# Kernel tuning notes

Measured on AMD Instinct MI355X. Metric: run time of the kernel, lower is better.

## Reference

```python
import jax, jax.numpy as jnp
import numpy as np

VOCAB = 10000
HID = 256

def setup_inputs() -> dict:
    key = jax.random.key(0)
    ks = jax.random.split(key, 7)
    B, T = 64, 64
    input_data = jax.random.randint(ks[0], (B, T), 0, VOCAB, dtype=jnp.int32)
    targets = jax.random.randint(ks[1], (B, T), 0, VOCAB, dtype=jnp.int32)
    # Xavier-ish scaled params
    E = jax.random.normal(ks[2], (VOCAB, HID), dtype=jnp.float32) * (1.0 / np.sqrt(HID))
    W_lstm = jax.random.normal(ks[3], (2 * HID, 4 * HID), dtype=jnp.float32) * (1.0 / np.sqrt(2 * HID))
    b_lstm = jnp.zeros((4 * HID,), dtype=jnp.float32)
    W_dense = jax.random.normal(ks[4], (HID, VOCAB), dtype=jnp.float32) * (1.0 / np.sqrt(HID))
    b_dense = jnp.zeros((VOCAB,), dtype=jnp.float32)
    return {"input_data": input_data, "targets": targets, "E": E,
            "W_lstm": W_lstm, "b_lstm": b_lstm, "W_dense": W_dense, "b_dense": b_dense}

def lstm_scan(xs, W, b, h0, c0):
    # xs: [T, B, H] time-major. TF LSTMCell: gates = [x,h]@W + b, order i,j,f,o, forget_bias=1.0
    def step(carry, x):
        h, c = carry
        gates = jnp.concatenate([x, h], axis=-1) @ W + b  # [B, 4H]
        i, j, f, o = jnp.split(gates, 4, axis=-1)
        c_new = jax.nn.sigmoid(f + 1.0) * c + jax.nn.sigmoid(i) * jnp.tanh(j)
        h_new = jax.nn.sigmoid(o) * jnp.tanh(c_new)
        return (h_new, c_new), h_new
    (hT, cT), hs = jax.lax.scan(step, (h0, c0), xs)
    return hs, (hT, cT)

def reference(input_data, targets, E, W_lstm, b_lstm, W_dense, b_dense):
    B, T = input_data.shape
    inputs = E[input_data]                       # [B, T, H] embedding lookup (no dropout: eval)
    xs = jnp.transpose(inputs, (1, 0, 2))        # [T, B, H]
    h0 = jnp.zeros((B, HID), dtype=E.dtype)
    c0 = jnp.zeros((B, HID), dtype=E.dtype)
    hs, _ = lstm_scan(xs, W_lstm, b_lstm, h0, c0)  # [T, B, H]
    outputs = jnp.transpose(hs, (1, 0, 2))       # [B, T, H]
    logits = outputs @ W_dense + b_dense         # [B, T, V]
    logp = jax.nn.log_softmax(logits, axis=-1)
    ce = -jnp.take_along_axis(logp, targets[..., None].astype(jnp.int32), axis=-1)[..., 0]  # [B, T]
    perplexity = jnp.exp(ce)                     # elementwise, as in add_loss_op
    return perplexity
```

## Files before the change

### kernel.cpp

```cpp
#include <hip/hip_runtime.h>
#include <math.h>

#define VOCABN 10000
#define HIDN   256
#define GATES  1024
#define BN     64
#define TN     64
#define BT     4096
#define NCT    625

typedef unsigned int       u32;
typedef unsigned short     u16;
typedef unsigned long long u64;
typedef float v4f __attribute__((ext_vector_type(4)));
typedef short v8s __attribute__((ext_vector_type(8)));

__device__ __forceinline__ float bf2f(u16 u) {
    return __uint_as_float(((u32)u) << 16);
}
__device__ __forceinline__ u16 f2bf(float f) {
    u32 u = __float_as_uint(f);
    u += 0x7FFFu + ((u >> 16) & 1u);
    return (u16)(u >> 16);
}
__device__ __forceinline__ float fast_sigmoid(float x) {
    return 1.0f / (1.0f + __expf(-x));
}
__device__ __forceinline__ float fast_tanh(float x) {
    float e = __expf(-2.0f * fabsf(x));
    float t = (1.0f - e) / (1.0f + e);
    return copysignf(t, x);
}
__device__ __forceinline__ u64 llc_load(const u64* p) {
    return __hip_atomic_load(p, __ATOMIC_RELAXED, __HIP_MEMORY_SCOPE_AGENT);
}
__device__ __forceinline__ void llc_store(u64* p, u64 v) {
    __hip_atomic_store(p, v, __ATOMIC_RELAXED, __HIP_MEMORY_SCOPE_AGENT);
}

__global__ __launch_bounds__(256) void k_wfrag(
    const float* __restrict__ src,
    u16*         __restrict__ dst,
    int ncols)
{
    __shared__ u16 lt[HIDN][16];
    const int c = blockIdx.x;
    const int t = threadIdx.x;
    const float* s = src + (size_t)t * ncols + c * 16;
    #pragma unroll
    for (int j4 = 0; j4 < 4; ++j4) {
        float4 v = *(const float4*)(s + j4 * 4);
        lt[t][j4*4+0] = f2bf(v.x);
        lt[t][j4*4+1] = f2bf(v.y);
        lt[t][j4*4+2] = f2bf(v.z);
        lt[t][j4*4+3] = f2bf(v.w);
    }
    __syncthreads();
    #pragma unroll
    for (int h = 0; h < 2; ++h) {
        int f = t + h * 256;
        int q = f >> 6, l = f & 63;
        int m = l & 15, kb = q * 32 + ((l >> 4) & 3) * 8;
        u32 w[4];
        #pragma unroll
        for (int j = 0; j < 4; ++j)
            w[j] = (u32)lt[kb + 2*j][m] | ((u32)lt[kb + 2*j + 1][m] << 16);
        *(uint4*)(dst + (((size_t)c * 8 + q) * 64 + l) * 8) =
            make_uint4(w[0], w[1], w[2], w[3]);
    }
}

__global__ __launch_bounds__(256) void k_xgates(
    const int*   __restrict__ idx,
    const float* __restrict__ E,
    const u16*   __restrict__ Wxf,
    const float* __restrict__ bl,
    float*       __restrict__ gx)
{
    const int r0   = blockIdx.x * 16;
    const int tid  = threadIdx.x;
    const int w    = tid >> 6, lane = tid & 63;
    const int m    = lane & 15, quad = lane >> 4;

    v8s a[8];
    {
        const float* e = E + (size_t)idx[r0 + m] * HIDN + quad * 8;
        #pragma unroll
        for (int q = 0; q < 8; ++q) {
            float4 x0 = *(const float4*)(e + q * 32);
            float4 x1 = *(const float4*)(e + q * 32 + 4);
            uint4 t4 = make_uint4(
                (u32)f2bf(x0.x) | ((u32)f2bf(x0.y) << 16),
                (u32)f2bf(x0.z) | ((u32)f2bf(x0.w) << 16),
                (u32)f2bf(x1.x) | ((u32)f2bf(x1.y) << 16),
                (u32)f2bf(x1.z) | ((u32)f2bf(x1.w) << 16));
            a[q] = *(v8s*)&t4;
        }
    }

    for (int c = w; c < GATES / 16; c += 4) {
        v4f acc = {0.f, 0.f, 0.f, 0.f};
        #pragma unroll
        for (int q = 0; q < 8; ++q) {
            v8s b = *(const v8s*)(Wxf + (((size_t)c * 8 + q) * 64 + lane) * 8);
            acc = __builtin_amdgcn_mfma_f32_16x16x32_bf16(a[q], b, acc, 0, 0, 0);
        }
        const int col = c * 16 + m;
        const float bv = bl[col];
        #pragma unroll
        for (int r = 0; r < 4; ++r)
            gx[(size_t)(r0 + quad * 4 + r) * GATES + col] = acc[r] + bv;
    }
}

__global__ __launch_bounds__(256) void k_plstm(
    const u16*   __restrict__ Whf,
    const float* __restrict__ gx,
    u16*                      Hx,
    u16*         __restrict__ Hb,
    u32*                      bar)
{
    __shared__ uint4 Wl4[4 * 512];
    __shared__ float gl[4][16][16];

    const int tid  = threadIdx.x;
    const int rg   = blockIdx.x >> 4;
    const int ns   = blockIdx.x & 15;
    const int u0   = ns * 16;
    const int w    = tid >> 6;
    const int lane = tid & 63;
    const int m    = lane & 15, kq = lane >> 4;

    {
        const uint4* src = (const uint4*)Whf;
        #pragma unroll
        for (int i = 0; i < 8; ++i) {
            int e  = tid + i * 256;
            int ct = e >> 9, off = e & 511;
            Wl4[e] = src[(size_t)(ct * 16 + ns) * 512 + off];
        }
    }
    {
        float* g0 = (float*)gl;
        #pragma unroll
        for (int j = 0; j < 4; ++j) g0[tid * 4 + j] = 0.0f;
    }
    __syncthreads();

    const u16* Wl = (const u16*)Wl4;

    const int r = tid >> 4, u = tid & 15;
    const int b = rg * 16 + r;
    const float* gxp = gx + (size_t)b * TN * GATES + u0 + u;
    u16* hbp = Hb + (size_t)b * TN * HIDN + u0 + u;
    const int hxw = b * HIDN + u0 + u;
    const int aoff = (rg * 16 + m) * HIDN + kq * 8;

    float cstate = 0.0f;
    float4 gxr;
    gxr.x = gxp[0]; gxr.y = gxp[256]; gxr.z = gxp[512]; gxr.w = gxp[768];

    for (int t = 0; t < TN; ++t) {
        float4 gxn = gxr;
        if (t + 1 < TN) {
            const float* p = gxp + (size_t)(t + 1) * GATES;
            gxn.x = p[0]; gxn.y = p[256]; gxn.z = p[512]; gxn.w = p[768];
        }

        if (t > 0) {
            const u64* hsrc = (const u64*)(Hx + (t & 1) * (BN * HIDN) + aoff);
            v4f acc = {0.f, 0.f, 0.f, 0.f};
            #pragma unroll
            for (int q = 0; q < 8; ++q) {
                union { u64 d[2]; v8s v; } av;
                av.d[0] = llc_load(hsrc + q * 8);
                av.d[1] = llc_load(hsrc + q * 8 + 1);
                v8s bf = *(const v8s*)(Wl + ((w * 8 + q) * 64 + lane) * 8);
                acc = __builtin_amdgcn_mfma_f32_16x16x32_bf16(av.v, bf, acc, 0, 0, 0);
            }
            #pragma unroll
            for (int rr = 0; rr < 4; ++rr)
                gl[w][kq * 4 + rr][m] = acc[rr];
        }
        __syncthreads();

        {
            float ai = gl[0][r][u] + gxr.x;
            float aj = gl[1][r][u] + gxr.y;
            float af = gl[2][r][u] + gxr.z;
            float ao = gl[3][r][u] + gxr.w;
            float ig = fast_sigmoid(ai);
            float fg = fast_sigmoid(af + 1.0f);
            float og = fast_sigmoid(ao);
            float jt = fast_tanh(aj);
            cstate = fg * cstate + ig * jt;
            float hn = og * fast_tanh(cstate);
            u32 hv = f2bf(hn);
            hbp[(size_t)t * HIDN] = (u16)hv;

            if (t + 1 < TN) {
                u32 p1 = __shfl_down(hv, 1);
                u32 p2 = __shfl_down(hv, 2);
                u32 p3 = __shfl_down(hv, 3);
                if ((tid & 3) == 0) {
                    u64 pk = (u64)(hv | (p1 << 16))
                           | ((u64)(p2 | (p3 << 16)) << 32);
                    u64* dst = (u64*)(Hx + (((t & 1) ^ 1) * (BN * HIDN)) + hxw);
                    llc_store(dst, pk);
                }
            }
        }

        if (t + 1 < TN) {
            __syncthreads();
            if (tid == 0) {
                __hip_atomic_fetch_add(&bar[rg * 64], 1u, __ATOMIC_RELAXED,
                                       __HIP_MEMORY_SCOPE_AGENT);
                u32 tgt = (u32)(t + 1) * 16u;
                while (__hip_atomic_load(&bar[rg * 64], __ATOMIC_RELAXED,
                                         __HIP_MEMORY_SCOPE_AGENT) < tgt)
                    __builtin_amdgcn_s_sleep(1);
            }
            __syncthreads();
        }
        gxr = gxn;
    }
}

__global__ __launch_bounds__(256, 1) void k_dense(
    const u16*   __restrict__ Hb,
    const u16*   __restrict__ Wf,
    const float* __restrict__ bd,
    float*       __restrict__ S)
{
    __shared__ float Sl[64];
    const int bid = blockIdx.x;
    const int hv  = bid & 3;
    const int rg  = bid >> 2;
    const int r0  = rg * 64;
    const int tid = threadIdx.x;
    const int w   = tid >> 6, lane = tid & 63;
    const int m   = lane & 15, kq = lane >> 4;

    if (tid < 64) Sl[tid] = 0.0f;

    v8s a[4][8];
    #pragma unroll
    for (int rt = 0; rt < 4; ++rt) {
        const u16* hrow = Hb + (size_t)(r0 + rt * 16 + m) * HIDN + kq * 8;
        #pragma unroll
        for (int q = 0; q < 8; ++q)
            a[rt][q] = *(const v8s*)(hrow + q * 32);
    }
    __syncthreads();

    float s[4][4] = {{0.f,0.f,0.f,0.f},{0.f,0.f,0.f,0.f},
                     {0.f,0.f,0.f,0.f},{0.f,0.f,0.f,0.f}};
    const int cbeg = (hv * NCT) >> 2;
    const int cend = ((hv + 1) * NCT) >> 2;
    for (int c = cbeg + w; c < cend; c += 4) {
        v4f acc[4] = {{0.f,0.f,0.f,0.f},{0.f,0.f,0.f,0.f},
                      {0.f,0.f,0.f,0.f},{0.f,0.f,0.f,0.f}};
        #pragma unroll
        for (int q = 0; q < 8; ++q) {
            v8s bq = *(const v8s*)(Wf + (((size_t)c * 8 + q) * 64 + lane) * 8);
            #pragma unroll
            for (int rt = 0; rt < 4; ++rt)
                acc[rt] = __builtin_amdgcn_mfma_f32_16x16x32_bf16(
                              a[rt][q], bq, acc[rt], 0, 0, 0);
        }
        const float bv = bd[c * 16 + m];
        #pragma unroll
        for (int rt = 0; rt < 4; ++rt)
            #pragma unroll
            for (int r = 0; r < 4; ++r)
                s[rt][r] += __expf(acc[rt][r] + bv);
    }

    #pragma unroll
    for (int rt = 0; rt < 4; ++rt)
        #pragma unroll
        for (int r = 0; r < 4; ++r)
            atomicAdd(&Sl[rt * 16 + kq * 4 + r], s[rt][r]);
    __syncthreads();
    if (tid < 64) S[(size_t)hv * BT + r0 + tid] = Sl[tid];
}

__global__ __launch_bounds__(256) void k_target(
    const u16*   __restrict__ Hb,
    const u16*   __restrict__ Wf,
    const float* __restrict__ bd,
    const int*   __restrict__ tgt,
    float*       __restrict__ tl)
{
    const int tid = threadIdx.x;
    const int row = blockIdx.x * 8 + (tid >> 5);
    const int t   = tid & 31;
    const int q   = t >> 2, lq = t & 3;
    const int v   = tgt[row];
    const int c   = v >> 4, vm = v & 15;
    const int kb  = q * 32 + lq * 8;

    v8s h  = *(const v8s*)(Hb + (size_t)row * HIDN + kb);
    v8s wv = *(const v8s*)(Wf + (((size_t)c * 8 + q) * 64 + lq * 16 + vm) * 8);
    float acc = 0.0f;
    #pragma unroll
    for (int j = 0; j < 8; ++j)
        acc = fmaf(bf2f((u16)h[j]), bf2f((u16)wv[j]), acc);
    #pragma unroll
    for (int off = 16; off >= 1; off >>= 1)
        acc += __shfl_down(acc, off, 32);
    if (t == 0) tl[row] = acc + bd[v];
}

__global__ __launch_bounds__(256) void k_final(
    const float* __restrict__ S,
    const float* __restrict__ tl,
    float*       __restrict__ out)
{
    int i = blockIdx.x * 256 + threadIdx.x;
    float sum = S[i] + S[BT + i] + S[2 * BT + i] + S[3 * BT + i];
    out[i] = __expf(__logf(sum) - tl[i]);
}

extern "C" void kernel_launch(void* const* d_in, const int* in_sizes, int n_in,
                              void* d_out, int out_size, void* d_ws, size_t ws_size,
                              hipStream_t stream) {
    const int*   input   = (const int*)  d_in[0];
    const int*   targets = (const int*)  d_in[1];
    const float* E       = (const float*)d_in[2];
    const float* W_lstm  = (const float*)d_in[3];
    const float* b_lstm  = (const float*)d_in[4];
    const float* W_dense = (const float*)d_in[5];
    const float* b_dense = (const float*)d_in[6];
    float* out = (float*)d_out;

    char* ws = (char*)d_ws;
    float* gx  = (float*)ws;
    u16*   Wf  = (u16*)ws;
    u16*   Hb  = (u16*)(ws + ((size_t)16 << 20));
    u16*   Whf = (u16*)(ws + ((size_t)18 << 20));
    u16*   Wxf = (u16*)(ws + ((size_t)18 << 20) + ((size_t)512 << 10));
    u16*   Hx  = (u16*)(ws + ((size_t)19 << 20));
    float* S   = (float*)(ws + ((size_t)19 << 20) + ((size_t)64 << 10));
    float* tl  = (float*)(ws + ((size_t)19 << 20) + ((size_t)128 << 10));
    u32*   bar = (u32*)  (ws + ((size_t)19 << 20) + ((size_t)144 << 10));

    hipMemsetAsync(bar, 0, 1024, stream);
    k_wfrag <<<64,      256, 0, stream>>>(W_lstm,                      Wxf, GATES);
    k_wfrag <<<64,      256, 0, stream>>>(W_lstm + (size_t)HIDN*GATES, Whf, GATES);
    k_xgates<<<BT / 16, 256, 0, stream>>>(input, E, Wxf, b_lstm, gx);
    k_plstm <<<64,      256, 0, stream>>>(Whf, gx, Hx, Hb, bar);
    k_wfrag <<<NCT,     256, 0, stream>>>(W_dense, Wf, VOCABN);
    k_dense <<<256,     256, 0, stream>>>(Hb, Wf, b_dense, S);
    k_target<<<BT / 8,  256, 0, stream>>>(Hb, Wf, b_dense, targets, tl);
    k_final <<<BT / 256,256, 0, stream>>>(S, tl, out);
}
```

Baseline: 384.8 us.

## Merge prologue and epilogue kernels using device-side counters to cut launches

The weight-fragment conversion and x-gate GEMM become one kernel, and the dense-weight conversion, dense log-sum-exp, target-logit extraction and final perplexity become a second kernel. Inside each, blocks wait on atomic completion counters instead of kernel boundaries. The target logit is taken from the dense MFMA tile rather than a separate dot-product kernel, and the last block per row group computes the output. This removes five launches and their gaps. In exchange it relies on spin-waiting, which can deadlock if the waiting blocks are scheduled before the producer blocks and fill the GPU.

```diff
diff --git a/kernel.cpp b/kernel.cpp
--- a/kernel.cpp
+++ b/kernel.cpp
@@ -37,15 +37,24 @@
 __device__ __forceinline__ void llc_store(u64* p, u64 v) {
     __hip_atomic_store(p, v, __ATOMIC_RELAXED, __HIP_MEMORY_SCOPE_AGENT);
 }
-
-__global__ __launch_bounds__(256) void k_wfrag(
-    const float* __restrict__ src,
-    u16*         __restrict__ dst,
-    int ncols)
+__device__ __forceinline__ float llc_loadf(const float* p) {
+    return __hip_atomic_load(p, __ATOMIC_RELAXED, __HIP_MEMORY_SCOPE_AGENT);
+}
+__device__ __forceinline__ void llc_storef(float* p, float v) {
+    __hip_atomic_store(p, v, __ATOMIC_RELAXED, __HIP_MEMORY_SCOPE_AGENT);
+}
+__device__ __forceinline__ u32 cnt_add(u32* p) {
+    return __hip_atomic_fetch_add(p, 1u, __ATOMIC_RELAXED,
+                                  __HIP_MEMORY_SCOPE_AGENT);
+}
+__device__ __forceinline__ u32 cnt_read(u32* p) {
+    return __hip_atomic_load(p, __ATOMIC_RELAXED, __HIP_MEMORY_SCOPE_AGENT);
+}
+
+__device__ __forceinline__ void wfrag_dev(
+    const float* __restrict__ src, u16* __restrict__ dst, int ncols, int c,
+    int t, u16 lt[HIDN][16])
 {
-    __shared__ u16 lt[HIDN][16];
-    const int c = blockIdx.x;
-    const int t = threadIdx.x;
     const float* s = src + (size_t)t * ncols + c * 16;
     #pragma unroll
     for (int j4 = 0; j4 < 4; ++j4) {
@@ -65,20 +74,42 @@
         #pragma unroll
         for (int j = 0; j < 4; ++j)
             w[j] = (u32)lt[kb + 2*j][m] | ((u32)lt[kb + 2*j + 1][m] << 16);
-        *(uint4*)(dst + (((size_t)c * 8 + q) * 64 + l) * 8) =
-            make_uint4(w[0], w[1], w[2], w[3]);
-    }
-}
-
-__global__ __launch_bounds__(256) void k_xgates(
+        u64* d = (u64*)(dst + (((size_t)c * 8 + q) * 64 + l) * 8);
+        llc_store(d,     (u64)w[0] | ((u64)w[1] << 32));
+        llc_store(d + 1, (u64)w[2] | ((u64)w[3] << 32));
+    }
+}
+
+__global__ __launch_bounds__(256) void k_pre(
+    const float* __restrict__ W_lstm,
     const int*   __restrict__ idx,
     const float* __restrict__ E,
-    const u16*   __restrict__ Wxf,
     const float* __restrict__ bl,
-    float*       __restrict__ gx)
+    u16*         __restrict__ Wxf,
+    u16*         __restrict__ Whf,
+    float*       __restrict__ gx,
+    u32*                      wxdone)
 {
-    const int r0   = blockIdx.x * 16;
-    const int tid  = threadIdx.x;
+    __shared__ u16 lt[HIDN][16];
+    const int bid = blockIdx.x;
+    const int tid = threadIdx.x;
+
+    if (bid < 64) {
+        wfrag_dev(W_lstm, Wxf, GATES, bid, tid, lt);
+        __syncthreads();
+        if (tid == 0) cnt_add(wxdone);
+        return;
+    }
+    if (bid < 128) {
+        wfrag_dev(W_lstm + (size_t)HIDN * GATES, Whf, GATES, bid - 64, tid, lt);
+        return;
+    }
+
+    if (tid == 0)
+        while (cnt_read(wxdone) < 64u) __builtin_amdgcn_s_sleep(8);
+    __syncthreads();
+
+    const int r0   = (bid - 128) * 16;
     const int w    = tid >> 6, lane = tid & 63;
     const int m    = lane & 15, quad = lane >> 4;
 
@@ -97,13 +128,14 @@
             a[q] = *(v8s*)&t4;
         }
     }
-
     for (int c = w; c < GATES / 16; c += 4) {
         v4f acc = {0.f, 0.f, 0.f, 0.f};
         #pragma unroll
         for (int q = 0; q < 8; ++q) {
-            v8s b = *(const v8s*)(Wxf + (((size_t)c * 8 + q) * 64 + lane) * 8);
-            acc = __builtin_amdgcn_mfma_f32_16x16x32_bf16(a[q], b, acc, 0, 0, 0);
+            union { u64 d[2]; v8s v; } bu;
+            const u64* bp = (const u64*)(Wxf + (((size_t)c * 8 + q) * 64 + lane) * 8);
+            bu.d[0] = bp[0]; bu.d[1] = bp[1];
+            acc = __builtin_amdgcn_mfma_f32_16x16x32_bf16(a[q], bu.v, acc, 0, 0, 0);
         }
         const int col = c * 16 + m;
         const float bv = bl[col];
@@ -214,11 +246,9 @@
         if (t + 1 < TN) {
             __syncthreads();
             if (tid == 0) {
-                __hip_atomic_fetch_add(&bar[rg * 64], 1u, __ATOMIC_RELAXED,
-                                       __HIP_MEMORY_SCOPE_AGENT);
+                cnt_add(&bar[rg * 64]);
                 u32 tgt = (u32)(t + 1) * 16u;
-                while (__hip_atomic_load(&bar[rg * 64], __ATOMIC_RELAXED,
-                                         __HIP_MEMORY_SCOPE_AGENT) < tgt)
+                while (cnt_read(&bar[rg * 64]) < tgt)
                     __builtin_amdgcn_s_sleep(1);
             }
             __syncthreads();
@@ -227,22 +257,43 @@
     }
 }
 
-__global__ __launch_bounds__(256, 1) void k_dense(
+__global__ __launch_bounds__(256, 1) void k_post(
+    const float* __restrict__ W_dense,
     const u16*   __restrict__ Hb,
-    const u16*   __restrict__ Wf,
+    u16*         __restrict__ Wf,
     const float* __restrict__ bd,
-    float*       __restrict__ S)
+    const int*   __restrict__ tgt,
+    float*                    S,
+    float*                    tl,
+    u32*                      wfdone,
+    u32*                      sdone,
+    float*       __restrict__ out)
 {
+    __shared__ u16   lt[HIDN][16];
     __shared__ float Sl[64];
+    __shared__ int   tg[64];
+
     const int bid = blockIdx.x;
-    const int hv  = bid & 3;
-    const int rg  = bid >> 2;
+    const int tid = threadIdx.x;
+
+    if (bid < NCT) {
+        wfrag_dev(W_dense, Wf, VOCABN, bid, tid, lt);
+        __syncthreads();
+        if (tid == 0) cnt_add(wfdone);
+        return;
+    }
+
+    const int db  = bid - NCT;
+    const int hv  = db & 3;
+    const int rg  = db >> 2;
     const int r0  = rg * 64;
-    const int tid = threadIdx.x;
     const int w   = tid >> 6, lane = tid & 63;
     const int m   = lane & 15, kq = lane >> 4;
 
-    if (tid < 64) Sl[tid] = 0.0f;
+    if (tid < 64) { Sl[tid] = 0.0f; tg[tid] = tgt[r0 + tid]; }
+    if (tid == 0)
+        while (cnt_read(wfdone) < (u32)NCT) __builtin_amdgcn_s_sleep(16);
+    __syncthreads();
 
     v8s a[4][8];
     #pragma unroll
@@ -252,7 +303,6 @@
         for (int q = 0; q < 8; ++q)
             a[rt][q] = *(const v8s*)(hrow + q * 32);
     }
-    __syncthreads();
 
     float s[4][4] = {{0.f,0.f,0.f,0.f},{0.f,0.f,0.f,0.f},
                      {0.f,0.f,0.f,0.f},{0.f,0.f,0.f,0.f}};
@@ -269,12 +319,17 @@
                 acc[rt] = __builtin_amdgcn_mfma_f32_16x16x32_bf16(
                               a[rt][q], bq, acc[rt], 0, 0, 0);
         }
-        const float bv = bd[c * 16 + m];
+        const int col = c * 16 + m;
+        const float bv = bd[col];
         #pragma unroll
         for (int rt = 0; rt < 4; ++rt)
             #pragma unroll
-            for (int r = 0; r < 4; ++r)
-                s[rt][r] += __expf(acc[rt][r] + bv);
+            for (int r = 0; r < 4; ++r) {
+                float l = acc[rt][r] + bv;
+                int row = rt * 16 + kq * 4 + r;
+                if (col == tg[row]) llc_storef(&tl[r0 + row], l);
+                s[rt][r] += __expf(l);
+            }
     }
 
     #pragma unroll
@@ -283,44 +338,18 @@
         for (int r = 0; r < 4; ++r)
             atomicAdd(&Sl[rt * 16 + kq * 4 + r], s[rt][r]);
     __syncthreads();
-    if (tid < 64) S[(size_t)hv * BT + r0 + tid] = Sl[tid];
-}
-
-__global__ __launch_bounds__(256) void k_target(
-    const u16*   __restrict__ Hb,
-    const u16*   __restrict__ Wf,
-    const float* __restrict__ bd,
-    const int*   __restrict__ tgt,
-    float*       __restrict__ tl)
-{
-    const int tid = threadIdx.x;
-    const int row = blockIdx.x * 8 + (tid >> 5);
-    const int t   = tid & 31;
-    const int q   = t >> 2, lq = t & 3;
-    const int v   = tgt[row];
-    const int c   = v >> 4, vm = v & 15;
-    const int kb  = q * 32 + lq * 8;
-
-    v8s h  = *(const v8s*)(Hb + (size_t)row * HIDN + kb);
-    v8s wv = *(const v8s*)(Wf + (((size_t)c * 8 + q) * 64 + lq * 16 + vm) * 8);
-    float acc = 0.0f;
-    #pragma unroll
-    for (int j = 0; j < 8; ++j)
-        acc = fmaf(bf2f((u16)h[j]), bf2f((u16)wv[j]), acc);
-    #pragma unroll
-    for (int off = 16; off >= 1; off >>= 1)
-        acc += __shfl_down(acc, off, 32);
-    if (t == 0) tl[row] = acc + bd[v];
-}
-
-__global__ __launch_bounds__(256) void k_final(
-    const float* __restrict__ S,
-    const float* __restrict__ tl,
-    float*       __restrict__ out)
-{
-    int i = blockIdx.x * 256 + threadIdx.x;
-    float sum = S[i] + S[BT + i] + S[2 * BT + i] + S[3 * BT + i];
-    out[i] = __expf(__logf(sum) - tl[i]);
+    if (tid < 64) atomicAdd(&S[r0 + tid], Sl[tid]);
+    __syncthreads();
+
+    if (tid == 0) Sl[0] = (float)cnt_add(&sdone[rg]);
+    __syncthreads();
+    if (Sl[0] == 3.0f) {
+        if (tid < 64) {
+            float sum = llc_loadf(&S[r0 + tid]);
+            float t   = llc_loadf(&tl[r0 + tid]);
+            out[r0 + tid] = __expf(__logf(sum) - t);
+        }
+    }
 }
 
 extern "C" void kernel_launch(void* const* d_in, const int* in_sizes, int n_in,
@@ -336,23 +365,24 @@
     float* out = (float*)d_out;
 
     char* ws = (char*)d_ws;
-    float* gx  = (float*)ws;
-    u16*   Wf  = (u16*)ws;
-    u16*   Hb  = (u16*)(ws + ((size_t)16 << 20));
-    u16*   Whf = (u16*)(ws + ((size_t)18 << 20));
-    u16*   Wxf = (u16*)(ws + ((size_t)18 << 20) + ((size_t)512 << 10));
-    u16*   Hx  = (u16*)(ws + ((size_t)19 << 20));
-    float* S   = (float*)(ws + ((size_t)19 << 20) + ((size_t)64 << 10));
-    float* tl  = (float*)(ws + ((size_t)19 << 20) + ((size_t)128 << 10));
-    u32*   bar = (u32*)  (ws + ((size_t)19 << 20) + ((size_t)144 << 10));
-
-    hipMemsetAsync(bar, 0, 1024, stream);
-    k_wfrag <<<64,      256, 0, stream>>>(W_lstm,                      Wxf, GATES);
-    k_wfrag <<<64,      256, 0, stream>>>(W_lstm + (size_t)HIDN*GATES, Whf, GATES);
-    k_xgates<<<BT / 16, 256, 0, stream>>>(input, E, Wxf, b_lstm, gx);
-    k_plstm <<<64,      256, 0, stream>>>(Whf, gx, Hx, Hb, bar);
-    k_wfrag <<<NCT,     256, 0, stream>>>(W_dense, Wf, VOCABN);
-    k_dense <<<256,     256, 0, stream>>>(Hb, Wf, b_dense, S);
-    k_target<<<BT / 8,  256, 0, stream>>>(Hb, Wf, b_dense, targets, tl);
-    k_final <<<BT / 256,256, 0, stream>>>(S, tl, out);
-}
+    float* gx     = (float*)ws;
+    u16*   Wf     = (u16*)ws;
+    u16*   Hb     = (u16*)(ws + ((size_t)16 << 20));
+    u16*   Whf    = (u16*)(ws + ((size_t)18 << 20));
+    u16*   Wxf    = (u16*)(ws + ((size_t)18 << 20) + ((size_t)512 << 10));
+    u16*   Hx     = (u16*)(ws + ((size_t)19 << 20));
+    float* S      = (float*)(ws + ((size_t)19 << 20) + ((size_t)64 << 10));
+    float* tl     = (float*)(ws + ((size_t)19 << 20) + ((size_t)80 << 10));
+    u32*   bar    = (u32*)  (ws + ((size_t)19 << 20) + ((size_t)96 << 10));
+    u32*   cnts   = (u32*)  (ws + ((size_t)19 << 20) + ((size_t)97 << 10));
+    u32*   wfdone = cnts;
+    u32*   wxdone = cnts + 1;
+    u32*   sdone  = cnts + 2;
+
+    hipMemsetAsync(S, 0, (size_t)34 << 10, stream);
+    k_pre  <<<384, 256, 0, stream>>>(W_lstm, input, E, b_lstm,
+                                     Wxf, Whf, gx, wxdone);
+    k_plstm<<<64,  256, 0, stream>>>(Whf, gx, Hx, Hb, bar);
+    k_post <<<NCT + 256, 256, 0, stream>>>(W_dense, Hb, Wf, b_dense, targets,
+                                           S, tl, wfdone, sdone, out);
+}
```

Result: slower. 467.7 us (+21.5%).
